# Optimization experiments

Measured on AMD Instinct MI355X. Metric: run time of the kernel, lower is better.

Reference implementation:

```python
import jax, jax.numpy as jnp
import numpy as np

B, T = 2, 1024
D_MODEL = 2048
D_STATE = 64            # N
HEADDIM = 64            # P (module sets headdim = d_state)
EXPAND = 2
D_CONV = 4
NGROUPS = 1
D_INNER = EXPAND * D_MODEL                     # 4096
NHEADS = D_INNER // HEADDIM                    # 64
CONV_DIM = D_INNER + 2 * NGROUPS * D_STATE     # 4224
D_IN_PROJ = 2 * D_INNER + 2 * NGROUPS * D_STATE + NHEADS  # 8384
EPS = 1e-5


def setup_inputs() -> dict:
    key = jax.random.key(0)
    k = jax.random.split(key, 10)
    n = lambda kk, sh, sc: jax.random.normal(kk, sh, jnp.float32) * sc
    return {
        "x": n(k[0], (B, T, D_MODEL), 1.0),
        "ln_w": jnp.ones((D_MODEL,), jnp.float32),
        "ln_b": jnp.zeros((D_MODEL,), jnp.float32),
        "in_proj_w": n(k[1], (D_IN_PROJ, D_MODEL), D_MODEL ** -0.5),
        "conv_w": n(k[2], (CONV_DIM, D_CONV), 0.5),
        "conv_b": n(k[3], (CONV_DIM,), 0.02),
        "dt_bias": n(k[4], (NHEADS,), 0.5),
        "A_log": jnp.log(jax.random.uniform(k[5], (NHEADS,), jnp.float32, 1.0, 16.0)),
        "D": 1.0 + n(k[6], (NHEADS,), 0.1),
        "norm_w": jnp.ones((D_INNER,), jnp.float32),
        "out_proj_w": n(k[7], (D_MODEL, D_INNER), D_INNER ** -0.5),
    }


def _layernorm(x, w, b):
    mu = x.mean(-1, keepdims=True)
    var = ((x - mu) ** 2).mean(-1, keepdims=True)
    return (x - mu) * jax.lax.rsqrt(var + EPS) * w + b


def _mamba2(u, in_proj_w, conv_w, conv_b, dt_bias, A_log, D, norm_w, out_proj_w):
    zxbcdt = u @ in_proj_w.T                         # [B,T,D_IN_PROJ]
    z = zxbcdt[..., :D_INNER]                        # gate
    xBC = zxbcdt[..., D_INNER:D_INNER + CONV_DIM]
    dt = zxbcdt[..., D_INNER + CONV_DIM:]            # [B,T,H]
    # causal depthwise conv1d (kernel size D_CONV) + SiLU
    xp = jnp.pad(xBC, ((0, 0), (D_CONV - 1, 0), (0, 0)))
    conv = conv_b
    for kk in range(D_CONV):
        conv = conv + xp[:, kk:kk + T, :] * conv_w[:, kk]
    xBC = jax.nn.silu(conv)
    x_in = xBC[..., :D_INNER].reshape(B, T, NHEADS, HEADDIM)   # [B,T,H,P]
    Bm = xBC[..., D_INNER:D_INNER + D_STATE]         # [B,T,N] (ngroups=1)
    Cm = xBC[..., D_INNER + D_STATE:]                # [B,T,N]
    dt = jax.nn.softplus(dt + dt_bias)               # [B,T,H]
    A = -jnp.exp(A_log)                              # [H]
    dA = jnp.exp(dt * A)                             # [B,T,H]
    dtx = dt[..., None] * x_in                       # [B,T,H,P]

    def step(h, inp):
        dA_t, dtx_t, B_t, C_t = inp
        # h: [B,H,P,N]
        h = h * dA_t[:, :, None, None] + dtx_t[..., None] * B_t[:, None, None, :]
        y = jnp.einsum('bhpn,bn->bhp', h, C_t)
        return h, y

    h0 = jnp.zeros((B, NHEADS, HEADDIM, D_STATE), u.dtype)
    xs = (jnp.moveaxis(dA, 1, 0), jnp.moveaxis(dtx, 1, 0),
          jnp.moveaxis(Bm, 1, 0), jnp.moveaxis(Cm, 1, 0))
    _, ys = jax.lax.scan(step, h0, xs)               # ys: [T,B,H,P]
    y = jnp.moveaxis(ys, 0, 1) + D[:, None] * x_in   # skip term D*x
    y = y.reshape(B, T, D_INNER)
    # gated RMSNorm (norm_before_gate=False): rmsnorm(y * silu(z)) * w
    y = y * jax.nn.silu(z)
    y = y * jax.lax.rsqrt((y * y).mean(-1, keepdims=True) + EPS) * norm_w
    return y @ out_proj_w.T                          # [B,T,D_MODEL]


def reference(x, ln_w, ln_b, in_proj_w, conv_w, conv_b, dt_bias, A_log, D, norm_w, out_proj_w):
    # pre-norm Mamba2 block with residual: x + Mamba2(LayerNorm(x))
    return x + _mamba2(_layernorm(x, ln_w, ln_b), in_proj_w, conv_w, conv_b,
                       dt_bias, A_log, D, norm_w, out_proj_w)
```

## Files before the change

kernel.cpp:

```cpp
#include <hip/hip_runtime.h>
#include <hip/hip_bf16.h>

#define Bdim 2
#define Tdim 1024
#define DMODEL 2048
#define DSTATE 64
#define HEADDIM 64
#define DCONV 4
#define DINNER 4096
#define NHEADS 64
#define CONVDIM 4224
#define DINPROJ 8384
#define NPAD 8448
#define MROWS (Bdim*Tdim)
#define QC 64
#define NCHUNK (Tdim/QC)

typedef __attribute__((ext_vector_type(8))) short bf16x8;
typedef __attribute__((ext_vector_type(4))) float f32x4;
typedef __attribute__((ext_vector_type(4))) unsigned short u16x4;
typedef __attribute__((ext_vector_type(8))) unsigned short u16x8;

#define GLB(p) ((const __attribute__((address_space(1))) void*)(p))
#define LDS(p) ((__attribute__((address_space(3))) void*)(p))

__device__ __forceinline__ unsigned short f2bf(float f) {
    unsigned int x = __builtin_bit_cast(unsigned int, f);
    x += 0x7fffu + ((x >> 16) & 1u);
    return (unsigned short)(x >> 16);
}
__device__ __forceinline__ float bf2f(unsigned int u16) {
    unsigned int x = u16 << 16;
    return __builtin_bit_cast(float, x);
}
__device__ __forceinline__ float siluf(float v) {
    return v / (1.f + expf(-v));
}

#define CVT_A4 (NPAD * DMODEL / 4)
#define CVT_B4 (DMODEL * DINNER / 4)
#define CVT_BLKS ((CVT_A4 + CVT_B4) / 256)
__global__ __launch_bounds__(256) void prep_k(const float* __restrict__ in_proj,
                                              const float* __restrict__ out_proj,
                                              unsigned short* __restrict__ win,
                                              unsigned short* __restrict__ wout,
                                              const float* __restrict__ x,
                                              const float* __restrict__ lw,
                                              const float* __restrict__ lb,
                                              unsigned short* __restrict__ u) {
    if (blockIdx.x < CVT_BLKS) {
        int idx = blockIdx.x * 256 + threadIdx.x;
        if (idx < CVT_A4) {
            int i4 = idx * 4;
            int row = i4 >> 11;
            u16x4 o;
            if (row < DINPROJ) {
                float4 v = *(const float4*)(in_proj + i4);
                o = (u16x4){f2bf(v.x), f2bf(v.y), f2bf(v.z), f2bf(v.w)};
            } else {
                o = (u16x4){0, 0, 0, 0};
            }
            *(u16x4*)(win + i4) = o;
        } else {
            int i4 = (idx - CVT_A4) * 4;
            float4 v = *(const float4*)(out_proj + i4);
            *(u16x4*)(wout + i4) = (u16x4){f2bf(v.x), f2bf(v.y), f2bf(v.z), f2bf(v.w)};
        }
        return;
    }
    int row = blockIdx.x - CVT_BLKS;
    const float* xr = x + (size_t)row * DMODEL;
    float4 v[2];
    float s = 0.f, s2 = 0.f;
#pragma unroll
    for (int i = 0; i < 2; ++i) {
        int c = (threadIdx.x + 256 * i) * 4;
        v[i] = *(const float4*)(xr + c);
        s += v[i].x + v[i].y + v[i].z + v[i].w;
        s2 += v[i].x * v[i].x + v[i].y * v[i].y + v[i].z * v[i].z + v[i].w * v[i].w;
    }
#pragma unroll
    for (int off = 32; off; off >>= 1) { s += __shfl_down(s, off); s2 += __shfl_down(s2, off); }
    __shared__ float rs[4], rs2[4];
    if ((threadIdx.x & 63) == 0) { rs[threadIdx.x >> 6] = s; rs2[threadIdx.x >> 6] = s2; }
    __syncthreads();
    s = rs[0] + rs[1] + rs[2] + rs[3];
    s2 = rs2[0] + rs2[1] + rs2[2] + rs2[3];
    float mu = s * (1.f / DMODEL);
    float var = s2 * (1.f / DMODEL) - mu * mu;
    float inv = rsqrtf(var + 1e-5f);
#pragma unroll
    for (int i = 0; i < 2; ++i) {
        int c = (threadIdx.x + 256 * i) * 4;
        float4 wv = *(const float4*)(lw + c);
        float4 bv = *(const float4*)(lb + c);
        u16x4 o = {f2bf((v[i].x - mu) * inv * wv.x + bv.x),
                   f2bf((v[i].y - mu) * inv * wv.y + bv.y),
                   f2bf((v[i].z - mu) * inv * wv.z + bv.z),
                   f2bf((v[i].w - mu) * inv * wv.w + bv.w)};
        *(u16x4*)(u + (size_t)row * DMODEL + c) = o;
    }
}

#define WAITV(n) asm volatile("s_waitcnt vmcnt(" #n ")" ::: "memory")
#define LGKM0   do { asm volatile("s_waitcnt lgkmcnt(0)" ::: "memory"); \
                     __builtin_amdgcn_sched_barrier(0); } while (0)
#define SCB     __builtin_amdgcn_sched_barrier(0)
#define BAR     __builtin_amdgcn_s_barrier()

template <int KTILES>
__global__ __launch_bounds__(512, 4) void gemm1_k32(const unsigned short* __restrict__ A,
                                                    const unsigned short* __restrict__ Bw,
                                                    float* __restrict__ Cout,
                                                    int N, int lda, int ldb,
                                                    int nb, int mb) {
    constexpr int BM = 256, BN = 128;
    __shared__ unsigned short As[2][BM * 32];
    __shared__ unsigned short Bs[2][BN * 32];

    const int bid = blockIdx.x;
    const int per_panel = mb * 8;
    const int fullp = (nb / 8) * per_panel;
    int mt, nt;
    if (bid < fullp) {
        int p = bid / per_panel, r = bid % per_panel;
        nt = p * 8 + r / mb; mt = r % mb;
    } else {
        int r = bid - fullp;
        nt = (nb / 8) * 8 + r / mb; mt = r % mb;
    }
    const int m0 = mt * BM, n0 = nt * BN;

    const int tid = threadIdx.x;
    const int lane = tid & 63, w = tid >> 6;
    const int wm = (w >> 1) * 64;
    const int wn = (w & 1) * 64;
    const int row16 = lane & 15, quad = lane >> 4;

    const unsigned short* gA[2];
    const unsigned short* gB0;
#pragma unroll
    for (int l = 0; l < 2; ++l) {
        int c = l * 512 + tid, rp = c >> 3, gp = (c & 7) ^ (rp & 7);
        int row = rp * 2 + (gp >> 2), kb = gp & 3;
        gA[l] = A + (size_t)(m0 + row) * lda + kb * 8;
    }
    {
        int c = tid, rp = c >> 3, gp = (c & 7) ^ (rp & 7);
        int row = rp * 2 + (gp >> 2), kb = gp & 3;
        gB0 = Bw + (size_t)(n0 + row) * ldb + kb * 8;
    }

    int aoff[4], boff[4];
#pragma unroll
    for (int i = 0; i < 4; ++i) {
        int row = wm + i * 16 + row16, rp = row >> 1;
        int s = (((row & 1) << 2) + quad) ^ (rp & 7);
        aoff[i] = rp * 64 + s * 8;
    }
#pragma unroll
    for (int j = 0; j < 4; ++j) {
        int row = wn + j * 16 + row16, rp = row >> 1;
        int s = (((row & 1) << 2) + quad) ^ (rp & 7);
        boff[j] = rp * 64 + s * 8;
    }

#define STG(d, kt) do {                                                            \
    __builtin_amdgcn_global_load_lds(GLB(gA[0] + (kt) * 32),                       \
                                     LDS(&As[d][tid * 8]), 16, 0, 0);              \
    __builtin_amdgcn_global_load_lds(GLB(gA[1] + (kt) * 32),                       \
                                     LDS(&As[d][(512 + tid) * 8]), 16, 0, 0);      \
    __builtin_amdgcn_global_load_lds(GLB(gB0 + (kt) * 32),                         \
                                     LDS(&Bs[d][tid * 8]), 16, 0, 0);              \
} while (0)

    f32x4 acc[4][4];
#pragma unroll
    for (int i = 0; i < 4; ++i)
#pragma unroll
        for (int j = 0; j < 4; ++j) acc[i][j] = (f32x4){0.f, 0.f, 0.f, 0.f};
    bf16x8 bfr[4], af[4];

    STG(0, 0);
    int cur = 0;
    for (int t = 0; t < KTILES; ++t) {
        if (t + 1 < KTILES) {
            STG(cur ^ 1, t + 1);
            WAITV(3);
        } else {
            WAITV(0);
        }
        BAR;
#pragma unroll
        for (int j = 0; j < 4; ++j) bfr[j] = *(const bf16x8*)&Bs[cur][boff[j]];
#pragma unroll
        for (int i = 0; i < 4; ++i) af[i] = *(const bf16x8*)&As[cur][aoff[i]];
        LGKM0;
        __builtin_amdgcn_s_setprio(1);
#pragma unroll
        for (int i = 0; i < 4; ++i)
#pragma unroll
            for (int j = 0; j < 4; ++j)
                acc[i][j] = __builtin_amdgcn_mfma_f32_16x16x32_bf16(af[i], bfr[j], acc[i][j], 0, 0, 0);
        __builtin_amdgcn_s_setprio(0);
        BAR;
        cur ^= 1;
    }

#pragma unroll
    for (int i = 0; i < 4; ++i)
#pragma unroll
        for (int j = 0; j < 4; ++j)
#pragma unroll
            for (int r = 0; r < 4; ++r) {
                int m = m0 + wm + i * 16 + quad * 4 + r;
                int n = n0 + wn + j * 16 + row16;
                Cout[(size_t)m * N + n] = acc[i][j][r];
            }
#undef STG
}

template <int EPI, int NT, int BM, int BN, int KTILES>
__global__ __launch_bounds__(NT, 4) void gemm_cr(const unsigned short* __restrict__ A,
                                                 const unsigned short* __restrict__ Bw,
                                                 float* __restrict__ Cout,
                                                 const float* __restrict__ resid,
                                                 int N, int lda, int ldb,
                                                 int nb, int mb) {
    constexpr int MW = NT / 128;
    constexpr int NA = BM * 64 / 8 / NT;
    constexpr int NB = BN * 64 / 8 / NT;
    constexpr int IM = BM / MW / 16;
    constexpr int IMH = IM / 2;
    constexpr int IN = BN / 2 / 16;

    __shared__ unsigned short As[2][BM * 64];
    __shared__ unsigned short Bs[2][BN * 64];

    const int bid = blockIdx.x;
    const int per_panel = mb * 8;
    const int fullp = (nb / 8) * per_panel;
    int mt, nt;
    if (bid < fullp) {
        int p = bid / per_panel, r = bid % per_panel;
        nt = p * 8 + r / mb; mt = r % mb;
    } else {
        int r = bid - fullp;
        nt = (nb / 8) * 8 + r / mb; mt = r % mb;
    }
    const int m0 = mt * BM, n0 = nt * BN;

    const int tid = threadIdx.x;
    const int lane = tid & 63, w = tid >> 6;
    const int wm = (w >> 1) * (BM / MW);
    const int wn = (w & 1) * (BN / 2);
    const int row16 = lane & 15, quad = lane >> 4;
    const int swz = row16 & 7;

    const unsigned short* gA[NA];
    const unsigned short* gB[NB];
#pragma unroll
    for (int l = 0; l < NA; ++l) {
        int c = l * NT + tid, r = c >> 3, kb = (c & 7) ^ (r & 7);
        gA[l] = A + (size_t)(m0 + r) * lda + kb * 8;
    }
#pragma unroll
    for (int l = 0; l < NB; ++l) {
        int c = l * NT + tid, r = c >> 3, kb = (c & 7) ^ (r & 7);
        gB[l] = Bw + (size_t)(n0 + r) * ldb + kb * 8;
    }

#define STG_A(d, kt) do { _Pragma("unroll")                                           \
    for (int _l = 0; _l < NA; ++_l)                                                   \
        __builtin_amdgcn_global_load_lds(GLB(gA[_l] + (kt) * 64),                     \
                LDS(&As[d][(_l * NT + tid) * 8]), 16, 0, 0); } while (0)
#define STG_B(d, kt) do { _Pragma("unroll")                                           \
    for (int _l = 0; _l < NB; ++_l)                                                   \
        __builtin_amdgcn_global_load_lds(GLB(gB[_l] + (kt) * 64),                     \
                LDS(&Bs[d][(_l * NT + tid) * 8]), 16, 0, 0); } while (0)
#define WAITN() do { if constexpr (NA == 2) WAITV(2); else WAITV(4); } while (0)
#define RD_B(d) do { _Pragma("unroll") for (int _j = 0; _j < IN; ++_j)                \
                     _Pragma("unroll") for (int _kc = 0; _kc < 2; ++_kc) {            \
                         int _row = wn + _j * 16 + row16;                             \
                         int _g = (_kc * 4 + quad) ^ swz;                             \
                         bfr[_j][_kc] = *(const bf16x8*)&Bs[d][(_row * 8 + _g) * 8];  \
                     } } while (0)
#define RD_A(d, h) do { _Pragma("unroll") for (int _i = 0; _i < IMH; ++_i)            \
                        _Pragma("unroll") for (int _kc = 0; _kc < 2; ++_kc) {         \
                            int _row = wm + ((h) * IMH + _i) * 16 + row16;            \
                            int _g = (_kc * 4 + quad) ^ swz;                          \
                            af[_i][_kc] = *(const bf16x8*)&As[d][(_row * 8 + _g) * 8];\
                        } } while (0)
#define MM(h) do { __builtin_amdgcn_s_setprio(1);                                     \
                   _Pragma("unroll") for (int _kc = 0; _kc < 2; ++_kc)                \
                   _Pragma("unroll") for (int _i = 0; _i < IMH; ++_i)                 \
                   _Pragma("unroll") for (int _j = 0; _j < IN; ++_j)                  \
                       acc[(h) * IMH + _i][_j] = __builtin_amdgcn_mfma_f32_16x16x32_bf16( \
                           af[_i][_kc], bfr[_j][_kc], acc[(h) * IMH + _i][_j], 0, 0, 0);  \
                   __builtin_amdgcn_s_setprio(0); } while (0)

    f32x4 acc[IM][IN];
#pragma unroll
    for (int i = 0; i < IM; ++i)
#pragma unroll
        for (int j = 0; j < IN; ++j) acc[i][j] = (f32x4){0.f, 0.f, 0.f, 0.f};
    bf16x8 bfr[IN][2], af[IMH][2];

    STG_A(0, 0); STG_B(0, 0);

    const int KI = KTILES / 2;
    for (int i = 0; i < KI; ++i) {
        const int k1 = 2 * i + 1, k2 = 2 * i + 2;
        const bool st2 = (k2 < KTILES);
        STG_A(1, k1);
        WAITN();
        BAR;
        RD_B(0); RD_A(0, 0);
        LGKM0;
        MM(0);
        BAR;
        RD_A(0, 1);
        STG_B(1, k1);
        BAR;
        LGKM0;
        MM(1);
        BAR;
        if (st2) {
            STG_A(0, k2);
            WAITN();
        } else {
            WAITV(0);
        }
        BAR;
        RD_B(1); RD_A(1, 0);
        LGKM0;
        MM(0);
        BAR;
        RD_A(1, 1);
        if (st2) STG_B(0, k2);
        BAR;
        LGKM0;
        MM(1);
        BAR;
    }

#pragma unroll
    for (int i = 0; i < IM; ++i)
#pragma unroll
        for (int j = 0; j < IN; ++j)
#pragma unroll
            for (int r = 0; r < 4; ++r) {
                int m = m0 + wm + i * 16 + quad * 4 + r;
                int n = n0 + wn + j * 16 + row16;
                float v = acc[i][j][r];
                if (EPI == 0)
                    Cout[(size_t)m * N + n] = v;
                else
                    Cout[(size_t)m * N + n] = resid[(size_t)m * N + n] + v;
            }
#undef STG_A
#undef STG_B
#undef WAITN
#undef RD_A
#undef RD_B
#undef MM
}

#define CONV_T (MROWS * CONVDIM / 4)
__global__ __launch_bounds__(256) void convdt_k(const float* __restrict__ zx,
                                                const float* __restrict__ cw,
                                                const float* __restrict__ cb,
                                                const float* __restrict__ dt_bias,
                                                const float* __restrict__ A_log,
                                                float* __restrict__ xin,
                                                float* __restrict__ bcf,
                                                float* __restrict__ dtf,
                                                float* __restrict__ dtAf) {
    int idx = blockIdx.x * 256 + threadIdx.x;
    if (idx < CONV_T) {
        int cg = idx % (CONVDIM / 4);
        int bt = idx / (CONVDIM / 4);
        int c = cg * 4;
        int t = bt & (Tdim - 1);
        const float* base = zx + (size_t)bt * NPAD + DINNER + c;
        float4 acc = *(const float4*)(cb + c);
#pragma unroll
        for (int kk = 0; kk < DCONV; ++kk) {
            int tt = t - 3 + kk;
            if (tt >= 0) {
                float4 v = *(const float4*)(base + (long)(kk - 3) * NPAD);
                acc.x += v.x * cw[(c + 0) * 4 + kk];
                acc.y += v.y * cw[(c + 1) * 4 + kk];
                acc.z += v.z * cw[(c + 2) * 4 + kk];
                acc.w += v.w * cw[(c + 3) * 4 + kk];
            }
        }
        float4 s = {siluf(acc.x), siluf(acc.y), siluf(acc.z), siluf(acc.w)};
        if (c < DINNER) *(float4*)(xin + (size_t)bt * DINNER + c) = s;
        else            *(float4*)(bcf + (size_t)bt * 128 + (c - DINNER)) = s;
    } else {
        int d4 = (idx - CONV_T) * 4;
        int bt = d4 >> 6;
        int h = d4 & 63;
        float4 raw = *(const float4*)(zx + (size_t)bt * NPAD + (DINNER + CONVDIM) + h);
        float4 bias = *(const float4*)(dt_bias + h);
        float4 al = *(const float4*)(A_log + h);
        float r[4] = {raw.x + bias.x, raw.y + bias.y, raw.z + bias.z, raw.w + bias.w};
        float A[4] = {-expf(al.x), -expf(al.y), -expf(al.z), -expf(al.w)};
        float4 dtv, dta;
        float* dtp = (float*)&dtv; float* dap = (float*)&dta;
#pragma unroll
        for (int j = 0; j < 4; ++j) {
            float dv = (r[j] > 20.f) ? r[j] : log1pf(expf(r[j]));
            dtp[j] = dv;
            dap[j] = dv * A[j];
        }
        *(float4*)(dtf + bt * 64 + h) = dtv;
        *(float4*)(dtAf + bt * 64 + h) = dta;
    }
}

__global__ __launch_bounds__(256) void chunk_state_k(const float* __restrict__ xin,
                                                     const float* __restrict__ bcf,
                                                     const float* __restrict__ dtf,
                                                     const float* __restrict__ dtAf,
                                                     float* __restrict__ Sst,
                                                     float* __restrict__ laq) {
    const int blk = blockIdx.x;
    const int c = blk & 15, h = (blk >> 4) & 63, b = blk >> 10;
    const int bt0 = b * Tdim + c * QC;
    const int tid = threadIdx.x;

    __shared__ float Bs[QC][68];
    __shared__ float Dx[QC][68];
    __shared__ float wsh[QC];

    if (tid < QC) {
        float v = dtAf[(bt0 + tid) * NHEADS + h];
#pragma unroll
        for (int d = 1; d < 64; d <<= 1) {
            float o = __shfl_up(v, d, 64);
            v += (tid >= d) ? o : 0.f;
        }
        float la63 = __shfl(v, 63, 64);
        wsh[tid] = expf(la63 - v);
        if (tid == 63) laq[blk] = la63;
    }
    __syncthreads();

    const int row = tid >> 2, q = tid & 3;
    {
        float m = wsh[row] * dtf[(bt0 + row) * NHEADS + h];
        const float* xr = xin + (size_t)(bt0 + row) * DINNER + h * 64 + q * 16;
        const float* br = bcf + (size_t)(bt0 + row) * 128 + q * 16;
#pragma unroll
        for (int j = 0; j < 4; ++j) {
            float4 xv = *(const float4*)(xr + j * 4);
            float4 bv = *(const float4*)(br + j * 4);
            *(float4*)&Dx[row][q * 16 + j * 4] = (float4){m * xv.x, m * xv.y, m * xv.z, m * xv.w};
            *(float4*)&Bs[row][q * 16 + j * 4] = bv;
        }
    }
    __syncthreads();

    const int p0 = (tid >> 4) * 4, n0 = (tid & 15) * 4;
    float acc[4][4] = {};
    for (int i = 0; i < QC; ++i) {
        float4 dv = *(const float4*)&Dx[i][p0];
        float4 bv = *(const float4*)&Bs[i][n0];
        float dva[4] = {dv.x, dv.y, dv.z, dv.w};
        float bva[4] = {bv.x, bv.y, bv.z, bv.w};
#pragma unroll
        for (int a = 0; a < 4; ++a)
#pragma unroll
            for (int e = 0; e < 4; ++e) acc[a][e] += dva[a] * bva[e];
    }
    float* Sp = Sst + (size_t)blk * NPAD;
#pragma unroll
    for (int a = 0; a < 4; ++a)
        *(float4*)&Sp[(p0 + a) * 64 + n0] = (float4){acc[a][0], acc[a][1], acc[a][2], acc[a][3]};
}

__global__ __launch_bounds__(256) void combine_k(float* __restrict__ Sst,
                                                 const float* __restrict__ laq) {
    const int bh = blockIdx.x >> 1;
    const int half = blockIdx.x & 1;
    const int tid = threadIdx.x;
    float4 r0 = {}, r1 = {};
    for (int c = 0; c < NCHUNK - 1; ++c) {
        float* p = Sst + (size_t)(bh * 16 + c) * NPAD + half * 2048 + tid * 8;
        float P = expf(laq[bh * 16 + c]);
        float4 s0 = ((const float4*)p)[0], s1 = ((const float4*)p)[1];
        r0 = (float4){P * r0.x + s0.x, P * r0.y + s0.y, P * r0.z + s0.z, P * r0.w + s0.w};
        r1 = (float4){P * r1.x + s1.x, P * r1.y + s1.y, P * r1.z + s1.z, P * r1.w + s1.w};
        ((float4*)p)[0] = r0; ((float4*)p)[1] = r1;
    }
}

__global__ __launch_bounds__(256) void chunk_out_k2(float* __restrict__ xin,
                                                    const float* __restrict__ bcf,
                                                    const float* __restrict__ dtf,
                                                    const float* __restrict__ dtAf,
                                                    const float* __restrict__ Sst,
                                                    const float* __restrict__ Dp) {
    const int blk = blockIdx.x;
    const int c = blk & 15, h = (blk >> 4) & 63, b = blk >> 10;
    const int bt0 = b * Tdim + c * QC;
    const int tid = threadIdx.x;

    __shared__ unsigned short Csh[64 * 64];
    __shared__ unsigned short Bsh[64 * 64];
    __shared__ unsigned short DxT[64 * 64];
    __shared__ unsigned short Gh [64 * 64];
    __shared__ unsigned short Hh [64 * 64];
    __shared__ float lash[QC];

    if (tid < QC) {
        float v = dtAf[(bt0 + tid) * NHEADS + h];
#pragma unroll
        for (int d = 1; d < 64; d <<= 1) {
            float o = __shfl_up(v, d, 64);
            v += (tid >= d) ? o : 0.f;
        }
        lash[tid] = v;
    }

    const int row = tid >> 2, q = tid & 3;
    {
        float m = dtf[(bt0 + row) * NHEADS + h];
        const float* xr = xin + (size_t)(bt0 + row) * DINNER + h * 64 + q * 16;
        const float* br = bcf + (size_t)(bt0 + row) * 128 + q * 16;
        const float* cr = bcf + (size_t)(bt0 + row) * 128 + 64 + q * 16;
        float xb[16];
        u16x8 cc[2], bb[2];
#pragma unroll
        for (int j = 0; j < 4; ++j) {
            float4 xv = *(const float4*)(xr + j * 4);
            float4 bv = *(const float4*)(br + j * 4);
            float4 cv = *(const float4*)(cr + j * 4);
            xb[j * 4 + 0] = m * xv.x; xb[j * 4 + 1] = m * xv.y;
            xb[j * 4 + 2] = m * xv.z; xb[j * 4 + 3] = m * xv.w;
            int hi = j >> 1, lo = (j & 1) * 4;
            cc[hi][lo + 0] = f2bf(cv.x); cc[hi][lo + 1] = f2bf(cv.y);
            cc[hi][lo + 2] = f2bf(cv.z); cc[hi][lo + 3] = f2bf(cv.w);
            bb[hi][lo + 0] = f2bf(bv.x); bb[hi][lo + 1] = f2bf(bv.y);
            bb[hi][lo + 2] = f2bf(bv.z); bb[hi][lo + 3] = f2bf(bv.w);
        }
        const int base = row * 64;
        const int c0 = ((q * 2) ^ (row & 7)) * 8, c1 = ((q * 2 + 1) ^ (row & 7)) * 8;
        *(u16x8*)&Csh[base + c0] = cc[0];  *(u16x8*)&Csh[base + c1] = cc[1];
        *(u16x8*)&Bsh[base + c0] = bb[0];  *(u16x8*)&Bsh[base + c1] = bb[1];
#pragma unroll
        for (int k2 = 0; k2 < 16; ++k2) {
            int p = q * 16 + k2;
            DxT[p * 64 + (((row >> 3) ^ (p & 7)) * 8 + (row & 7))] = f2bf(xb[k2]);
        }
        if (c > 0) {
            const float* Hp = Sst + (size_t)(blk - 1) * NPAD + row * 64 + q * 16;
            u16x8 hh[2];
#pragma unroll
            for (int j = 0; j < 4; ++j) {
                float4 hv = *(const float4*)(Hp + j * 4);
                int hi = j >> 1, lo = (j & 1) * 4;
                hh[hi][lo + 0] = f2bf(hv.x); hh[hi][lo + 1] = f2bf(hv.y);
                hh[hi][lo + 2] = f2bf(hv.z); hh[hi][lo + 3] = f2bf(hv.w);
            }
            *(u16x8*)&Hh[base + c0] = hh[0];  *(u16x8*)&Hh[base + c1] = hh[1];
        }
    }
    __syncthreads();

    const int lane = tid & 63, w = tid >> 6;
    const int t0 = w * 16;
    const int row16 = lane & 15, quad = lane >> 4;
    const int swz = row16 & 7;

    f32x4 a1[4];
#pragma unroll
    for (int st = 0; st < 4; ++st) a1[st] = (f32x4){0.f, 0.f, 0.f, 0.f};
#pragma unroll
    for (int kc = 0; kc < 2; ++kc) {
        int g = ((kc * 4 + quad) ^ swz) * 8;
        bf16x8 ca = *(const bf16x8*)&Csh[(t0 + row16) * 64 + g];
#pragma unroll
        for (int st = 0; st < 4; ++st) {
            bf16x8 bs = *(const bf16x8*)&Bsh[(st * 16 + row16) * 64 + g];
            a1[st] = __builtin_amdgcn_mfma_f32_16x16x32_bf16(ca, bs, a1[st], 0, 0, 0);
        }
    }
    float latv[4];
#pragma unroll
    for (int r = 0; r < 4; ++r) latv[r] = lash[t0 + quad * 4 + r];
#pragma unroll
    for (int st = 0; st < 4; ++st) {
        int s = st * 16 + row16;
        float las = lash[s];
#pragma unroll
        for (int r = 0; r < 4; ++r) {
            int t = t0 + quad * 4 + r;
            float gv = (s <= t) ? a1[st][r] * expf(latv[r] - las) : 0.f;
            Gh[t * 64 + (((s >> 3) ^ (t & 7)) * 8 + (s & 7))] = f2bf(gv);
        }
    }
    __syncthreads();

    f32x4 aS[4], aH[4];
#pragma unroll
    for (int pt = 0; pt < 4; ++pt) { aS[pt] = (f32x4){0.f,0.f,0.f,0.f}; aH[pt] = (f32x4){0.f,0.f,0.f,0.f}; }
#pragma unroll
    for (int kc = 0; kc < 2; ++kc) {
        int g = ((kc * 4 + quad) ^ swz) * 8;
        bf16x8 ga = *(const bf16x8*)&Gh[(t0 + row16) * 64 + g];
#pragma unroll
        for (int pt = 0; pt < 4; ++pt) {
            bf16x8 db = *(const bf16x8*)&DxT[(pt * 16 + row16) * 64 + g];
            aS[pt] = __builtin_amdgcn_mfma_f32_16x16x32_bf16(ga, db, aS[pt], 0, 0, 0);
        }
        if (c > 0) {
            bf16x8 ca = *(const bf16x8*)&Csh[(t0 + row16) * 64 + g];
#pragma unroll
            for (int pt = 0; pt < 4; ++pt) {
                bf16x8 hb = *(const bf16x8*)&Hh[(pt * 16 + row16) * 64 + g];
                aH[pt] = __builtin_amdgcn_mfma_f32_16x16x32_bf16(ca, hb, aH[pt], 0, 0, 0);
            }
        }
    }

    float Dh = Dp[h];
    float eA[4];
#pragma unroll
    for (int r = 0; r < 4; ++r) eA[r] = expf(latv[r]);
#pragma unroll
    for (int pt = 0; pt < 4; ++pt)
#pragma unroll
        for (int r = 0; r < 4; ++r) {
            int t = t0 + quad * 4 + r, p = pt * 16 + row16;
            float* xr2 = xin + (size_t)(bt0 + t) * DINNER + h * 64 + p;
            float xv = *xr2;
            float y = aS[pt][r] + Dh * xv;
            if (c > 0) y += eA[r] * aH[pt][r];
            *xr2 = y;
        }
}

__global__ __launch_bounds__(256) void gate_k(const float* __restrict__ ybf,
                                              const float* __restrict__ zx,
                                              const float* __restrict__ nw,
                                              unsigned short* __restrict__ yg,
                                              int ldyg) {
    int row = blockIdx.x;
    float4 tv[4];
    float s2 = 0.f;
#pragma unroll
    for (int i = 0; i < 4; ++i) {
        int c = (threadIdx.x + 256 * i) * 4;
        float4 y = *(const float4*)(ybf + (size_t)row * DINNER + c);
        float4 z = *(const float4*)(zx + (size_t)row * NPAD + c);
        float4 t = {y.x * siluf(z.x), y.y * siluf(z.y), y.z * siluf(z.z), y.w * siluf(z.w)};
        tv[i] = t;
        s2 += t.x * t.x + t.y * t.y + t.z * t.z + t.w * t.w;
    }
#pragma unroll
    for (int off = 32; off; off >>= 1) s2 += __shfl_down(s2, off);
    __shared__ float rs[4];
    if ((threadIdx.x & 63) == 0) rs[threadIdx.x >> 6] = s2;
    __syncthreads();
    s2 = rs[0] + rs[1] + rs[2] + rs[3];
    float scale = rsqrtf(s2 * (1.f / DINNER) + 1e-5f);
#pragma unroll
    for (int i = 0; i < 4; ++i) {
        int c = (threadIdx.x + 256 * i) * 4;
        float4 w = *(const float4*)(nw + c);
        u16x4 o = {f2bf(tv[i].x * scale * w.x), f2bf(tv[i].y * scale * w.y),
                   f2bf(tv[i].z * scale * w.z), f2bf(tv[i].w * scale * w.w)};
        *(u16x4*)(yg + (size_t)row * ldyg + c) = o;
    }
}

extern "C" void kernel_launch(void* const* d_in, const int* in_sizes, int n_in,
                              void* d_out, int out_size, void* d_ws, size_t ws_size,
                              hipStream_t stream) {
    const float* x        = (const float*)d_in[0];
    const float* ln_w     = (const float*)d_in[1];
    const float* ln_b     = (const float*)d_in[2];
    const float* in_proj  = (const float*)d_in[3];
    const float* conv_w   = (const float*)d_in[4];
    const float* conv_b   = (const float*)d_in[5];
    const float* dt_bias  = (const float*)d_in[6];
    const float* A_log    = (const float*)d_in[7];
    const float* Dp       = (const float*)d_in[8];
    const float* norm_w   = (const float*)d_in[9];
    const float* out_proj = (const float*)d_in[10];
    float* out = (float*)d_out;
    char* ws = (char*)d_ws;

    float*          zx   = (float*)(ws + 0);
    unsigned short* wout = (unsigned short*)(ws + 69206016);
    unsigned short* win  = (unsigned short*)(ws + 85983232);
    unsigned short* ubf  = (unsigned short*)(ws + 120586240);
    float*          xin  = (float*)(ws + 85983232);
    float*          bcf  = (float*)(ws + 120586240);
    float*          dtf  = (float*)(ws + 121634816);
    float*          dtAf = (float*)(ws + 122159104);
    float*          laq  = (float*)(ws + 122683392);
    float*          Sst  = zx + 4096;
    unsigned short* yg   = (unsigned short*)zx + 8192;
    const int       ldyg = 16896;

    prep_k<<<CVT_BLKS + MROWS, 256, 0, stream>>>(in_proj, out_proj, win, wout,
                                                 x, ln_w, ln_b, ubf);
    gemm1_k32<64><<<66 * 8, 512, 0, stream>>>(ubf, win, zx, NPAD, DMODEL, DMODEL, 66, 8);
    convdt_k<<<(CONV_T + MROWS * NHEADS / 4) / 256, 256, 0, stream>>>(zx, conv_w, conv_b,
                                                                      dt_bias, A_log,
                                                                      xin, bcf, dtf, dtAf);
    chunk_state_k<<<Bdim * NHEADS * NCHUNK, 256, 0, stream>>>(xin, bcf, dtf, dtAf, Sst, laq);
    combine_k<<<2 * Bdim * NHEADS, 256, 0, stream>>>(Sst, laq);
    chunk_out_k2<<<Bdim * NHEADS * NCHUNK, 256, 0, stream>>>(xin, bcf, dtf, dtAf, Sst, Dp);
    gate_k<<<MROWS, 256, 0, stream>>>(xin, zx, norm_w, yg, ldyg);
    gemm_cr<1, 256, 128, 64, 64><<<32 * 16, 256, 0, stream>>>(yg, wout, out, x,
                                                              DMODEL, ldyg, DINNER, 32, 16);
}
```

Before: 463.6 us.

## Triple-buffer in-proj GEMM, slide conv window, MFMA chunk state, widen out-proj

The in-projection GEMM moves from a double to a triple LDS buffer with a prefetch distance of two tiles, to hide global-load latency. The conv kernel now has each thread walk a 32-step time segment with a sliding register window, so every input row is loaded once instead of four times. The chunk-state outer product switches from fp32 FMAs to bf16 MFMA with swizzled transposed LDS tiles, which lowers precision of the states. The out-projection GEMM now runs with 512 threads per block instead of 256, at the same tile size.

```diff
diff --git a/kernel.cpp b/kernel.cpp
--- a/kernel.cpp
+++ b/kernel.cpp
@@ -109,14 +109,14 @@
 #define BAR     __builtin_amdgcn_s_barrier()
 
 template <int KTILES>
-__global__ __launch_bounds__(512, 4) void gemm1_k32(const unsigned short* __restrict__ A,
-                                                    const unsigned short* __restrict__ Bw,
-                                                    float* __restrict__ Cout,
-                                                    int N, int lda, int ldb,
-                                                    int nb, int mb) {
+__global__ __launch_bounds__(512, 4) void gemm1_w8(const unsigned short* __restrict__ A,
+                                                   const unsigned short* __restrict__ Bw,
+                                                   float* __restrict__ Cout,
+                                                   int N, int lda, int ldb,
+                                                   int nb, int mb) {
     constexpr int BM = 256, BN = 128;
-    __shared__ unsigned short As[2][BM * 32];
-    __shared__ unsigned short Bs[2][BN * 32];
+    __shared__ unsigned short As[3][BM * 32];
+    __shared__ unsigned short Bs[3][BN * 32];
 
     const int bid = blockIdx.x;
     const int per_panel = mb * 8;
@@ -181,20 +181,26 @@
         for (int j = 0; j < 4; ++j) acc[i][j] = (f32x4){0.f, 0.f, 0.f, 0.f};
     bf16x8 bfr[4], af[4];
 
-    STG(0, 0);
-    int cur = 0;
+    STG(0, 0); STG(1, 1);
+
+    int bc = 0;
     for (int t = 0; t < KTILES; ++t) {
-        if (t + 1 < KTILES) {
-            STG(cur ^ 1, t + 1);
+        int bn2 = bc + 2; if (bn2 >= 3) bn2 -= 3;
+        if (t + 2 < KTILES) {
+            STG(bn2, t + 2);
+            WAITV(6);
+        } else if (t + 1 < KTILES) {
             WAITV(3);
         } else {
             WAITV(0);
         }
         BAR;
-#pragma unroll
-        for (int j = 0; j < 4; ++j) bfr[j] = *(const bf16x8*)&Bs[cur][boff[j]];
-#pragma unroll
-        for (int i = 0; i < 4; ++i) af[i] = *(const bf16x8*)&As[cur][aoff[i]];
+        const unsigned short* Ab = As[bc];
+        const unsigned short* Bb = Bs[bc];
+#pragma unroll
+        for (int j = 0; j < 4; ++j) bfr[j] = *(const bf16x8*)&Bb[boff[j]];
+#pragma unroll
+        for (int i = 0; i < 4; ++i) af[i] = *(const bf16x8*)&Ab[aoff[i]];
         LGKM0;
         __builtin_amdgcn_s_setprio(1);
 #pragma unroll
@@ -204,7 +210,7 @@
                 acc[i][j] = __builtin_amdgcn_mfma_f32_16x16x32_bf16(af[i], bfr[j], acc[i][j], 0, 0, 0);
         __builtin_amdgcn_s_setprio(0);
         BAR;
-        cur ^= 1;
+        bc = bc + 1; if (bc == 3) bc = 0;
     }
 
 #pragma unroll
@@ -220,19 +226,18 @@
 #undef STG
 }
 
-template <int EPI, int NT, int BM, int BN, int KTILES>
-__global__ __launch_bounds__(NT, 4) void gemm_cr(const unsigned short* __restrict__ A,
-                                                 const unsigned short* __restrict__ Bw,
-                                                 float* __restrict__ Cout,
-                                                 const float* __restrict__ resid,
-                                                 int N, int lda, int ldb,
-                                                 int nb, int mb) {
-    constexpr int MW = NT / 128;
-    constexpr int NA = BM * 64 / 8 / NT;
-    constexpr int NB = BN * 64 / 8 / NT;
-    constexpr int IM = BM / MW / 16;
+template <int EPI, int BM, int BN, int KTILES>
+__global__ __launch_bounds__(512, 4) void gemm_cr(const unsigned short* __restrict__ A,
+                                                  const unsigned short* __restrict__ Bw,
+                                                  float* __restrict__ Cout,
+                                                  const float* __restrict__ resid,
+                                                  int N, int lda, int ldb,
+                                                  int nb, int mb) {
+    constexpr int NA = BM / 64;
+    constexpr int NB = BN / 64;
+    constexpr int IM = BM / 64;
     constexpr int IMH = IM / 2;
-    constexpr int IN = BN / 2 / 16;
+    constexpr int IN = BN / 32;
 
     __shared__ unsigned short As[2][BM * 64];
     __shared__ unsigned short Bs[2][BN * 64];
@@ -252,7 +257,7 @@
 
     const int tid = threadIdx.x;
     const int lane = tid & 63, w = tid >> 6;
-    const int wm = (w >> 1) * (BM / MW);
+    const int wm = (w >> 1) * (BM / 4);
     const int wn = (w & 1) * (BN / 2);
     const int row16 = lane & 15, quad = lane >> 4;
     const int swz = row16 & 7;
@@ -261,23 +266,23 @@
     const unsigned short* gB[NB];
 #pragma unroll
     for (int l = 0; l < NA; ++l) {
-        int c = l * NT + tid, r = c >> 3, kb = (c & 7) ^ (r & 7);
+        int c = l * 512 + tid, r = c >> 3, kb = (c & 7) ^ (r & 7);
         gA[l] = A + (size_t)(m0 + r) * lda + kb * 8;
     }
 #pragma unroll
     for (int l = 0; l < NB; ++l) {
-        int c = l * NT + tid, r = c >> 3, kb = (c & 7) ^ (r & 7);
+        int c = l * 512 + tid, r = c >> 3, kb = (c & 7) ^ (r & 7);
         gB[l] = Bw + (size_t)(n0 + r) * ldb + kb * 8;
     }
 
 #define STG_A(d, kt) do { _Pragma("unroll")                                           \
     for (int _l = 0; _l < NA; ++_l)                                                   \
         __builtin_amdgcn_global_load_lds(GLB(gA[_l] + (kt) * 64),                     \
-                LDS(&As[d][(_l * NT + tid) * 8]), 16, 0, 0); } while (0)
+                LDS(&As[d][(_l * 512 + tid) * 8]), 16, 0, 0); } while (0)
 #define STG_B(d, kt) do { _Pragma("unroll")                                           \
     for (int _l = 0; _l < NB; ++_l)                                                   \
         __builtin_amdgcn_global_load_lds(GLB(gB[_l] + (kt) * 64),                     \
-                LDS(&Bs[d][(_l * NT + tid) * 8]), 16, 0, 0); } while (0)
+                LDS(&Bs[d][(_l * 512 + tid) * 8]), 16, 0, 0); } while (0)
 #define WAITN() do { if constexpr (NA == 2) WAITV(2); else WAITV(4); } while (0)
 #define RD_B(d) do { _Pragma("unroll") for (int _j = 0; _j < IN; ++_j)                \
                      _Pragma("unroll") for (int _kc = 0; _kc < 2; ++_kc) {            \
@@ -366,40 +371,57 @@
 #undef MM
 }
 
-#define CONV_T (MROWS * CONVDIM / 4)
-__global__ __launch_bounds__(256) void convdt_k(const float* __restrict__ zx,
-                                                const float* __restrict__ cw,
-                                                const float* __restrict__ cb,
-                                                const float* __restrict__ dt_bias,
-                                                const float* __restrict__ A_log,
-                                                float* __restrict__ xin,
-                                                float* __restrict__ bcf,
-                                                float* __restrict__ dtf,
-                                                float* __restrict__ dtAf) {
-    int idx = blockIdx.x * 256 + threadIdx.x;
-    if (idx < CONV_T) {
-        int cg = idx % (CONVDIM / 4);
-        int bt = idx / (CONVDIM / 4);
+#define CGRP (CONVDIM / 4)
+#define TSEG 32
+#define SEGS (Tdim / TSEG)
+#define CPART 5
+#define CONV_BLKS (Bdim * SEGS * CPART)
+#define DT_BLKS (MROWS * NHEADS / 4 / 256)
+__global__ __launch_bounds__(256) void convdt2_k(const float* __restrict__ zx,
+                                                 const float* __restrict__ cw,
+                                                 const float* __restrict__ cb,
+                                                 const float* __restrict__ dt_bias,
+                                                 const float* __restrict__ A_log,
+                                                 float* __restrict__ xin,
+                                                 float* __restrict__ bcf,
+                                                 float* __restrict__ dtf,
+                                                 float* __restrict__ dtAf) {
+    int blk = blockIdx.x;
+    if (blk < CONV_BLKS) {
+        int part = blk % CPART;
+        int seg  = (blk / CPART) % SEGS;
+        int b    = blk / (CPART * SEGS);
+        int cg = part * 256 + threadIdx.x;
+        if (cg >= CGRP) return;
         int c = cg * 4;
-        int t = bt & (Tdim - 1);
-        const float* base = zx + (size_t)bt * NPAD + DINNER + c;
-        float4 acc = *(const float4*)(cb + c);
-#pragma unroll
-        for (int kk = 0; kk < DCONV; ++kk) {
-            int tt = t - 3 + kk;
-            if (tt >= 0) {
-                float4 v = *(const float4*)(base + (long)(kk - 3) * NPAD);
-                acc.x += v.x * cw[(c + 0) * 4 + kk];
-                acc.y += v.y * cw[(c + 1) * 4 + kk];
-                acc.z += v.z * cw[(c + 2) * 4 + kk];
-                acc.w += v.w * cw[(c + 3) * 4 + kk];
-            }
-        }
-        float4 s = {siluf(acc.x), siluf(acc.y), siluf(acc.z), siluf(acc.w)};
-        if (c < DINNER) *(float4*)(xin + (size_t)bt * DINNER + c) = s;
-        else            *(float4*)(bcf + (size_t)bt * 128 + (c - DINNER)) = s;
+        float4 k0 = {cw[(c + 0) * 4 + 0], cw[(c + 1) * 4 + 0], cw[(c + 2) * 4 + 0], cw[(c + 3) * 4 + 0]};
+        float4 k1 = {cw[(c + 0) * 4 + 1], cw[(c + 1) * 4 + 1], cw[(c + 2) * 4 + 1], cw[(c + 3) * 4 + 1]};
+        float4 k2 = {cw[(c + 0) * 4 + 2], cw[(c + 1) * 4 + 2], cw[(c + 2) * 4 + 2], cw[(c + 3) * 4 + 2]};
+        float4 k3 = {cw[(c + 0) * 4 + 3], cw[(c + 1) * 4 + 3], cw[(c + 2) * 4 + 3], cw[(c + 3) * 4 + 3]};
+        float4 bias = *(const float4*)(cb + c);
+        const int t0 = seg * TSEG;
+        const float* bp = zx + (size_t)(b * Tdim) * NPAD + DINNER + c;
+        float4 w0 = {0.f, 0.f, 0.f, 0.f}, w1 = w0, w2 = w0;
+        if (t0 - 3 >= 0) w0 = *(const float4*)(bp + (size_t)(t0 - 3) * NPAD);
+        if (t0 - 2 >= 0) w1 = *(const float4*)(bp + (size_t)(t0 - 2) * NPAD);
+        if (t0 - 1 >= 0) w2 = *(const float4*)(bp + (size_t)(t0 - 1) * NPAD);
+#pragma unroll 4
+        for (int t = t0; t < t0 + TSEG; ++t) {
+            float4 w3 = *(const float4*)(bp + (size_t)t * NPAD);
+            float4 a;
+            a.x = bias.x + w0.x * k0.x + w1.x * k1.x + w2.x * k2.x + w3.x * k3.x;
+            a.y = bias.y + w0.y * k0.y + w1.y * k1.y + w2.y * k2.y + w3.y * k3.y;
+            a.z = bias.z + w0.z * k0.z + w1.z * k1.z + w2.z * k2.z + w3.z * k3.z;
+            a.w = bias.w + w0.w * k0.w + w1.w * k1.w + w2.w * k2.w + w3.w * k3.w;
+            float4 s = {siluf(a.x), siluf(a.y), siluf(a.z), siluf(a.w)};
+            int bt = b * Tdim + t;
+            if (c < DINNER) *(float4*)(xin + (size_t)bt * DINNER + c) = s;
+            else            *(float4*)(bcf + (size_t)bt * 128 + (c - DINNER)) = s;
+            w0 = w1; w1 = w2; w2 = w3;
+        }
     } else {
-        int d4 = (idx - CONV_T) * 4;
+        int idx = (blk - CONV_BLKS) * 256 + threadIdx.x;
+        int d4 = idx * 4;
         int bt = d4 >> 6;
         int h = d4 & 63;
         float4 raw = *(const float4*)(zx + (size_t)bt * NPAD + (DINNER + CONVDIM) + h);
@@ -420,19 +442,19 @@
     }
 }
 
-__global__ __launch_bounds__(256) void chunk_state_k(const float* __restrict__ xin,
-                                                     const float* __restrict__ bcf,
-                                                     const float* __restrict__ dtf,
-                                                     const float* __restrict__ dtAf,
-                                                     float* __restrict__ Sst,
-                                                     float* __restrict__ laq) {
+__global__ __launch_bounds__(256) void chunk_state_k2(const float* __restrict__ xin,
+                                                      const float* __restrict__ bcf,
+                                                      const float* __restrict__ dtf,
+                                                      const float* __restrict__ dtAf,
+                                                      float* __restrict__ Sst,
+                                                      float* __restrict__ laq) {
     const int blk = blockIdx.x;
     const int c = blk & 15, h = (blk >> 4) & 63, b = blk >> 10;
     const int bt0 = b * Tdim + c * QC;
     const int tid = threadIdx.x;
 
-    __shared__ float Bs[QC][68];
-    __shared__ float Dx[QC][68];
+    __shared__ unsigned short DxT2[64 * 64];
+    __shared__ unsigned short BT2 [64 * 64];
     __shared__ float wsh[QC];
 
     if (tid < QC) {
@@ -457,28 +479,45 @@
         for (int j = 0; j < 4; ++j) {
             float4 xv = *(const float4*)(xr + j * 4);
             float4 bv = *(const float4*)(br + j * 4);
-            *(float4*)&Dx[row][q * 16 + j * 4] = (float4){m * xv.x, m * xv.y, m * xv.z, m * xv.w};
-            *(float4*)&Bs[row][q * 16 + j * 4] = bv;
+            float xa[4] = {m * xv.x, m * xv.y, m * xv.z, m * xv.w};
+            float ba[4] = {bv.x, bv.y, bv.z, bv.w};
+#pragma unroll
+            for (int k2 = 0; k2 < 4; ++k2) {
+                int p = q * 16 + j * 4 + k2;
+                int off = p * 64 + (((row >> 3) ^ (p & 7)) << 3) + (row & 7);
+                DxT2[off] = f2bf(xa[k2]);
+                BT2[off]  = f2bf(ba[k2]);
+            }
         }
     }
     __syncthreads();
 
-    const int p0 = (tid >> 4) * 4, n0 = (tid & 15) * 4;
-    float acc[4][4] = {};
-    for (int i = 0; i < QC; ++i) {
-        float4 dv = *(const float4*)&Dx[i][p0];
-        float4 bv = *(const float4*)&Bs[i][n0];
-        float dva[4] = {dv.x, dv.y, dv.z, dv.w};
-        float bva[4] = {bv.x, bv.y, bv.z, bv.w};
-#pragma unroll
-        for (int a = 0; a < 4; ++a)
-#pragma unroll
-            for (int e = 0; e < 4; ++e) acc[a][e] += dva[a] * bva[e];
+    const int lane = tid & 63, w = tid >> 6;
+    const int t0 = w * 16;
+    const int row16 = lane & 15, quad = lane >> 4;
+    const int swz = row16 & 7;
+
+    f32x4 aS[4];
+#pragma unroll
+    for (int nt = 0; nt < 4; ++nt) aS[nt] = (f32x4){0.f, 0.f, 0.f, 0.f};
+#pragma unroll
+    for (int kc = 0; kc < 2; ++kc) {
+        int g = ((kc * 4 + quad) ^ swz) * 8;
+        bf16x8 ga = *(const bf16x8*)&DxT2[(t0 + row16) * 64 + g];
+#pragma unroll
+        for (int nt = 0; nt < 4; ++nt) {
+            bf16x8 bs = *(const bf16x8*)&BT2[(nt * 16 + row16) * 64 + g];
+            aS[nt] = __builtin_amdgcn_mfma_f32_16x16x32_bf16(ga, bs, aS[nt], 0, 0, 0);
+        }
     }
     float* Sp = Sst + (size_t)blk * NPAD;
 #pragma unroll
-    for (int a = 0; a < 4; ++a)
-        *(float4*)&Sp[(p0 + a) * 64 + n0] = (float4){acc[a][0], acc[a][1], acc[a][2], acc[a][3]};
+    for (int nt = 0; nt < 4; ++nt)
+#pragma unroll
+        for (int r = 0; r < 4; ++r) {
+            int p = t0 + quad * 4 + r, n = nt * 16 + row16;
+            Sp[p * 64 + n] = aS[nt][r];
+        }
 }
 
 __global__ __launch_bounds__(256) void combine_k(float* __restrict__ Sst,
@@ -709,14 +748,14 @@
 
     prep_k<<<CVT_BLKS + MROWS, 256, 0, stream>>>(in_proj, out_proj, win, wout,
                                                  x, ln_w, ln_b, ubf);
-    gemm1_k32<64><<<66 * 8, 512, 0, stream>>>(ubf, win, zx, NPAD, DMODEL, DMODEL, 66, 8);
-    convdt_k<<<(CONV_T + MROWS * NHEADS / 4) / 256, 256, 0, stream>>>(zx, conv_w, conv_b,
-                                                                      dt_bias, A_log,
-                                                                      xin, bcf, dtf, dtAf);
-    chunk_state_k<<<Bdim * NHEADS * NCHUNK, 256, 0, stream>>>(xin, bcf, dtf, dtAf, Sst, laq);
+    gemm1_w8<64><<<66 * 8, 512, 0, stream>>>(ubf, win, zx, NPAD, DMODEL, DMODEL, 66, 8);
+    convdt2_k<<<CONV_BLKS + DT_BLKS, 256, 0, stream>>>(zx, conv_w, conv_b,
+                                                       dt_bias, A_log,
+                                                       xin, bcf, dtf, dtAf);
+    chunk_state_k2<<<Bdim * NHEADS * NCHUNK, 256, 0, stream>>>(xin, bcf, dtf, dtAf, Sst, laq);
     combine_k<<<2 * Bdim * NHEADS, 256, 0, stream>>>(Sst, laq);
     chunk_out_k2<<<Bdim * NHEADS * NCHUNK, 256, 0, stream>>>(xin, bcf, dtf, dtAf, Sst, Dp);
     gate_k<<<MROWS, 256, 0, stream>>>(xin, zx, norm_w, yg, ldyg);
-    gemm_cr<1, 256, 128, 64, 64><<<32 * 16, 256, 0, stream>>>(yg, wout, out, x,
-                                                              DMODEL, ldyg, DINNER, 32, 16);
-}
+    gemm_cr<1, 128, 64, 64><<<32 * 16, 512, 0, stream>>>(yg, wout, out, x,
+                                                         DMODEL, ldyg, DINNER, 32, 16);
+}
```

Result: faster. 412.1 us (-11.1%).
